# Optimization experiments

Measured on AMD Instinct MI355X. Metric: run time of the kernel, lower is better.

Reference implementation:

```python
import jax, jax.numpy as jnp
import numpy as np

TEMPERATURE = 0.07
BASE_TEMPERATURE = 0.07


def _supcon_one(feat, labels):
    # feat: [B, V, D], labels: [B]  (contrast_mode='all')
    B, V, D = feat.shape
    N = V * B
    # torch.cat(torch.unbind(feat, dim=1), dim=0): view-major ordering
    contrast = jnp.swapaxes(feat, 0, 1).reshape(N, D)  # [N, D]
    logits = jnp.einsum('nd,md->nm', contrast, contrast) / TEMPERATURE  # [N, N]
    # subtract detached row max for numerical stability
    logits = logits - jax.lax.stop_gradient(jnp.max(logits, axis=1, keepdims=True))
    pos = (labels[:, None] == labels[None, :]).astype(feat.dtype)  # [B, B]
    mask = jnp.tile(pos, (V, V))                                   # [N, N]
    logits_mask = 1.0 - jnp.eye(N, dtype=feat.dtype)               # zero out self-contrast
    mask = mask * logits_mask
    exp_logits = jnp.exp(logits) * logits_mask
    log_prob = logits - jnp.log(exp_logits.sum(axis=1, keepdims=True))
    mean_log_prob_pos = (mask * log_prob).sum(axis=1) / mask.sum(axis=1)
    return -(TEMPERATURE / BASE_TEMPERATURE) * mean_log_prob_pos.mean()


def setup_inputs() -> dict:
    key = jax.random.key(0)
    k1, k2 = jax.random.split(key)
    feat = jax.random.normal(k1, (16, 1024, 2, 128), dtype=jnp.float32)
    feat = feat / jnp.linalg.norm(feat, axis=-1, keepdims=True)  # unit-norm embeddings
    labels = jax.random.randint(k2, (16, 1024), 0, 64)
    return {"features": feat, "labels": labels}


def reference(features, labels):
    # vmap over the outer batch dim (replaces the Python loop), then mean
    losses = jax.vmap(_supcon_one)(features, labels)
    return losses.mean()
```

## Files before the change

kernel.cpp:

```cpp
#include <hip/hip_runtime.h>
#include <hip/hip_bf16.h>

#define TEMP_INV 14.285714285714286f
#define KL2E     20.60992947626f
#define NC2      (-20.60992947626f)
#define NBATCH 16
#define NROWS 2048
#define DDIM 128

typedef __attribute__((ext_vector_type(8))) short bf16x8;
typedef __attribute__((ext_vector_type(4))) float f32x4;

#define GLOAD16(g, l) \
  __builtin_amdgcn_global_load_lds((const __attribute__((address_space(1))) void*)(g), \
                                   (__attribute__((address_space(3))) void*)(l), 16, 0, 0)

__global__ __launch_bounds__(256) void cast_reorder_kernel(
    const float* __restrict__ feat, __hip_bfloat16* __restrict__ out)
{
    int t = blockIdx.x * blockDim.x + threadIdx.x;
    int e = t << 2;
    int d = e & 127;
    int v = (e >> 7) & 1;
    int i = (e >> 8) & 1023;
    int b = e >> 18;
    const float4 f = *reinterpret_cast<const float4*>(feat + e);
    union { __hip_bfloat16 h[4]; uint2 u; } o;
    o.h[0] = __float2bfloat16(f.x);
    o.h[1] = __float2bfloat16(f.y);
    o.h[2] = __float2bfloat16(f.z);
    o.h[3] = __float2bfloat16(f.w);
    size_t oe = (size_t)(((b << 11) + (v << 10) + i)) * DDIM + d;
    *reinterpret_cast<uint2*>(out + oe) = o.u;
}

__global__ __launch_bounds__(256) void supcon_main_kernel(
    const __hip_bfloat16* __restrict__ contrast,
    const int* __restrict__ labels,
    float* __restrict__ rsum_ws, float* __restrict__ ps_ws, float* __restrict__ sd_ws)
{
    __shared__ __hip_bfloat16 Bt[2][128 * DDIM];
    __shared__ int slab[1024];
    __shared__ float red_se[2][64], red_ps[2][64], red_sd[2][64];

    const int tid  = threadIdx.x;
    const int lane = tid & 63;
    const int w    = tid >> 6;
    const int wrow = w >> 1, wcol = w & 1;

    const int bid = blockIdx.x;
    const int xcd = bid & 7, idx = bid >> 3;
    const int b   = xcd * 2 + (idx >> 5);
    const int rb  = idx & 31;
    const int n0  = rb * 64;

    const __hip_bfloat16* cb = contrast + (size_t)b * NROWS * DDIM;
    const int* lb = labels + b * 1024;

    #pragma unroll
    for (int it = 0; it < 4; ++it) slab[it * 256 + tid] = lb[it * 256 + tid];

    #pragma unroll
    for (int c = 0; c < 4; ++c) {
        const int r = (c * 4 + w) * 4 + (lane >> 4);
        const int p = lane & 15;
        GLOAD16(cb + (size_t)(n0 + r) * DDIM + ((p ^ (r & 7)) << 3),
                (char*)(&Bt[1][0]) + (c * 4 + w) * 1024);
    }
    #pragma unroll
    for (int c = 0; c < 8; ++c) {
        const int r = (c * 4 + w) * 4 + (lane >> 4);
        const int p = lane & 15;
        GLOAD16(cb + (size_t)r * DDIM + ((p ^ (r & 7)) << 3),
                (char*)(&Bt[0][0]) + (c * 4 + w) * 1024);
    }
    __syncthreads();

    bf16x8 afrag[2][4];
    #pragma unroll
    for (int fr = 0; fr < 2; ++fr) {
        const int arow = wrow * 32 + fr * 16 + (lane & 15);
        #pragma unroll
        for (int ks = 0; ks < 4; ++ks) {
            const int q = ks * 4 + (lane >> 4);
            afrag[fr][ks] = *reinterpret_cast<const bf16x8*>(
                (const char*)(&Bt[1][0]) + arow * 256 + ((q ^ (arow & 7)) << 4));
        }
    }
    int rown[2][4], rowlab[2][4];
    #pragma unroll
    for (int fr = 0; fr < 2; ++fr)
        #pragma unroll
        for (int j = 0; j < 4; ++j) {
            const int n = n0 + wrow * 32 + fr * 16 + ((lane >> 4) << 2) + j;
            rown[fr][j] = n;
            rowlab[fr][j] = slab[n & 1023];
        }
    __syncthreads();

    const __hip_bfloat16* gsrc[8];
    #pragma unroll
    for (int c = 0; c < 8; ++c) {
        const int r = (c * 4 + w) * 4 + (lane >> 4);
        const int p = lane & 15;
        gsrc[c] = cb + (size_t)(128 + r) * DDIM + ((p ^ (r & 7)) << 3);
    }
    int boff[4][4];
    #pragma unroll
    for (int fc = 0; fc < 4; ++fc) {
        const int brow = wcol * 64 + fc * 16 + (lane & 15);
        #pragma unroll
        for (int ks = 0; ks < 4; ++ks) {
            const int q = ks * 4 + (lane >> 4);
            boff[fc][ks] = brow * 256 + ((q ^ (brow & 7)) << 4);
        }
    }

    float se[2][4] = {{0,0,0,0},{0,0,0,0}};
    float ps[2][4] = {{0,0,0,0},{0,0,0,0}};
    float sd[2][4] = {{0,0,0,0},{0,0,0,0}};
    const int tdiag = rb >> 1;

    for (int t = 0; t < 16; ++t) {
        const int cur = t & 1;
        if (t < 15) {
            #pragma unroll
            for (int c = 0; c < 8; ++c) {
                GLOAD16(gsrc[c], (char*)(&Bt[cur ^ 1][0]) + (c * 4 + w) * 1024);
                gsrc[c] += 128 * DDIM;
            }
        }
        const char* base = (const char*)(&Bt[cur][0]);

        f32x4 acc[2][4];
        #pragma unroll
        for (int fr = 0; fr < 2; ++fr)
            #pragma unroll
            for (int fc = 0; fc < 4; ++fc)
                acc[fr][fc] = (f32x4){0.f, 0.f, 0.f, 0.f};

        #pragma unroll
        for (int ks = 0; ks < 4; ++ks) {
            bf16x8 bfrag[4];
            #pragma unroll
            for (int fc = 0; fc < 4; ++fc)
                bfrag[fc] = *reinterpret_cast<const bf16x8*>(base + boff[fc][ks]);
            #pragma unroll
            for (int fr = 0; fr < 2; ++fr)
                #pragma unroll
                for (int fc = 0; fc < 4; ++fc)
                    acc[fr][fc] = __builtin_amdgcn_mfma_f32_16x16x32_bf16(
                        afrag[fr][ks], bfrag[fc], acc[fr][fc], 0, 0, 0);
        }

        const int m0 = t * 128;
        #pragma unroll
        for (int fc = 0; fc < 4; ++fc) {
            const int m = m0 + wcol * 64 + fc * 16 + (lane & 15);
            const int lm = slab[m & 1023];
            #pragma unroll
            for (int fr = 0; fr < 2; ++fr)
                #pragma unroll
                for (int j = 0; j < 4; ++j) {
                    const float val = acc[fr][fc][j];
                    se[fr][j] += exp2f(fmaf(val, KL2E, NC2));
                    ps[fr][j] += (lm == rowlab[fr][j]) ? val : 0.f;
                }
        }
        if (t == tdiag) {
            #pragma unroll
            for (int fc = 0; fc < 4; ++fc) {
                const int m = m0 + wcol * 64 + fc * 16 + (lane & 15);
                #pragma unroll
                for (int fr = 0; fr < 2; ++fr)
                    #pragma unroll
                    for (int j = 0; j < 4; ++j)
                        if (m == rown[fr][j]) sd[fr][j] = acc[fr][fc][j];
            }
        }
        __syncthreads();
    }

    #pragma unroll
    for (int fr = 0; fr < 2; ++fr)
        #pragma unroll
        for (int j = 0; j < 4; ++j) {
            float s = se[fr][j], P = ps[fr][j], D = sd[fr][j];
            #pragma unroll
            for (int o = 1; o < 16; o <<= 1) {
                s += __shfl_xor(s, o);
                P += __shfl_xor(P, o);
                D += __shfl_xor(D, o);
            }
            if ((lane & 15) == 0) {
                const int r = wrow * 32 + fr * 16 + ((lane >> 4) << 2) + j;
                red_se[wcol][r] = s; red_ps[wcol][r] = P; red_sd[wcol][r] = D;
            }
        }
    __syncthreads();
    if (tid < 64) {
        const int gn = b * NROWS + n0 + tid;
        rsum_ws[gn] = red_se[0][tid] + red_se[1][tid];
        ps_ws[gn]   = red_ps[0][tid] + red_ps[1][tid];
        sd_ws[gn]   = red_sd[0][tid] + red_sd[1][tid];
    }
}

__global__ __launch_bounds__(256) void finalize_kernel(
    const int* __restrict__ labels,
    const float* __restrict__ rsum_ws, const float* __restrict__ ps_ws,
    const float* __restrict__ sd_ws, float* __restrict__ out)
{
    __shared__ int cnt_s[64];
    __shared__ float wred[4];
    const int tid = threadIdx.x, lane = tid & 63, wv = tid >> 6;
    const int gid = blockIdx.x * 256 + tid;
    const int b = gid >> 11, n = gid & 2047;
    const int* lb = labels + b * 1024;

    if (tid < 64) cnt_s[tid] = 0;
    __syncthreads();
    #pragma unroll
    for (int k = 0; k < 4; ++k) atomicAdd(&cnt_s[lb[tid * 4 + k]], 1);
    __syncthreads();

    const int l = lb[n & 1023];
    const float poscnt = (float)(2 * cnt_s[l] - 1);
    const float D  = sd_ws[gid];
    const float P  = ps_ws[gid] - D;
    const float rs = rsum_ws[gid] - exp2f(fmaf(D, KL2E, NC2));
    float mlpp = P * TEMP_INV / poscnt - TEMP_INV - __logf(rs);

    #pragma unroll
    for (int o = 1; o < 64; o <<= 1) mlpp += __shfl_xor(mlpp, o);
    if (lane == 0) wred[wv] = mlpp;
    __syncthreads();
    if (tid == 0)
        atomicAdd(out, -(wred[0] + wred[1] + wred[2] + wred[3]) * (1.0f / 32768.0f));
}

extern "C" void kernel_launch(void* const* d_in, const int* in_sizes, int n_in,
                              void* d_out, int out_size, void* d_ws, size_t ws_size,
                              hipStream_t stream) {
    const float* feat = (const float*)d_in[0];
    const int* labels = (const int*)d_in[1];
    float* out = (float*)d_out;

    char* ws = (char*)d_ws;
    __hip_bfloat16* contrast = (__hip_bfloat16*)ws;
    float* rsum_ws = (float*)(ws + 8388608);
    float* ps_ws   = (float*)(ws + 8519680);
    float* sd_ws   = (float*)(ws + 8650752);

    hipMemsetAsync(d_out, 0, sizeof(float), stream);
    cast_reorder_kernel<<<4096, 256, 0, stream>>>(feat, contrast);
    supcon_main_kernel<<<512, 256, 0, stream>>>(contrast, labels, rsum_ws, ps_ws, sd_ws);
    finalize_kernel<<<128, 256, 0, stream>>>(labels, rsum_ws, ps_ws, sd_ws, out);
}
```

Measured before the change: 112.1 us.

## Split column range across blocks with per-wave private LDS streaming and atomic reduction

The main kernel is reorganized so each wave owns 16 rows and streams 16-column B tiles through its own private double-buffered LDS region. This removes block-wide __syncthreads from the inner loop. The column range is split into two halves across blocks, doubling the grid to 1024 blocks, and launch bounds now request higher occupancy. Partial row sums are combined with global atomics into a workspace that is zeroed by an extra memset. The cost is lower MFMA reuse per B fragment (one row tile per wave instead of 2x4), plus more global loads and atomics.

```diff
diff --git a/kernel.cpp b/kernel.cpp
--- a/kernel.cpp
+++ b/kernel.cpp
@@ -4,7 +4,6 @@
 #define TEMP_INV 14.285714285714286f
 #define KL2E     20.60992947626f
 #define NC2      (-20.60992947626f)
-#define NBATCH 16
 #define NROWS 2048
 #define DDIM 128
 
@@ -34,175 +33,130 @@
     *reinterpret_cast<uint2*>(out + oe) = o.u;
 }
 
-__global__ __launch_bounds__(256) void supcon_main_kernel(
+__global__ __launch_bounds__(256, 4) void supcon_main_kernel(
     const __hip_bfloat16* __restrict__ contrast,
     const int* __restrict__ labels,
     float* __restrict__ rsum_ws, float* __restrict__ ps_ws, float* __restrict__ sd_ws)
 {
-    __shared__ __hip_bfloat16 Bt[2][128 * DDIM];
+    __shared__ __align__(16) char wbuf[4][2][4096];
     __shared__ int slab[1024];
-    __shared__ float red_se[2][64], red_ps[2][64], red_sd[2][64];
 
     const int tid  = threadIdx.x;
     const int lane = tid & 63;
     const int w    = tid >> 6;
-    const int wrow = w >> 1, wcol = w & 1;
+    const int hi   = lane >> 4;
+    const int lo   = lane & 15;
 
     const int bid = blockIdx.x;
     const int xcd = bid & 7, idx = bid >> 3;
-    const int b   = xcd * 2 + (idx >> 5);
-    const int rb  = idx & 31;
+    const int b   = xcd * 2 + (idx >> 6);
+    const int rem = idx & 63;
+    const int rb  = rem >> 1, ch = rem & 1;
     const int n0  = rb * 64;
-
-    const __hip_bfloat16* cb = contrast + (size_t)b * NROWS * DDIM;
+    const int wr0 = n0 + w * 16;
+    const int cb0 = ch * 1024;
+
+    const __hip_bfloat16* cbase = contrast + (size_t)b * NROWS * DDIM;
     const int* lb = labels + b * 1024;
 
     #pragma unroll
     for (int it = 0; it < 4; ++it) slab[it * 256 + tid] = lb[it * 256 + tid];
 
-    #pragma unroll
-    for (int c = 0; c < 4; ++c) {
-        const int r = (c * 4 + w) * 4 + (lane >> 4);
-        const int p = lane & 15;
-        GLOAD16(cb + (size_t)(n0 + r) * DDIM + ((p ^ (r & 7)) << 3),
-                (char*)(&Bt[1][0]) + (c * 4 + w) * 1024);
-    }
-    #pragma unroll
-    for (int c = 0; c < 8; ++c) {
-        const int r = (c * 4 + w) * 4 + (lane >> 4);
-        const int p = lane & 15;
-        GLOAD16(cb + (size_t)r * DDIM + ((p ^ (r & 7)) << 3),
-                (char*)(&Bt[0][0]) + (c * 4 + w) * 1024);
-    }
-    __syncthreads();
-
-    bf16x8 afrag[2][4];
-    #pragma unroll
-    for (int fr = 0; fr < 2; ++fr) {
-        const int arow = wrow * 32 + fr * 16 + (lane & 15);
-        #pragma unroll
-        for (int ks = 0; ks < 4; ++ks) {
-            const int q = ks * 4 + (lane >> 4);
-            afrag[fr][ks] = *reinterpret_cast<const bf16x8*>(
-                (const char*)(&Bt[1][0]) + arow * 256 + ((q ^ (arow & 7)) << 4));
-        }
-    }
-    int rown[2][4], rowlab[2][4];
-    #pragma unroll
-    for (int fr = 0; fr < 2; ++fr)
+    char* buf0 = &wbuf[w][0][0];
+
+    #pragma unroll
+    for (int i = 0; i < 4; ++i) {
+        const int r = 4 * i + hi;
+        GLOAD16(cbase + (size_t)(wr0 + r) * DDIM + ((lo ^ (r & 7)) << 3),
+                buf0 + i * 1024);
+    }
+    asm volatile("s_waitcnt vmcnt(0)" ::: "memory");
+    __builtin_amdgcn_sched_barrier(0);
+
+    bf16x8 afrag[4];
+    int boff[4];
+    #pragma unroll
+    for (int ks = 0; ks < 4; ++ks) {
+        boff[ks] = lo * 256 + (((hi + 4 * ks) ^ (lo & 7)) << 4);
+        afrag[ks] = *reinterpret_cast<const bf16x8*>(buf0 + boff[ks]);
+    }
+    __syncthreads();
+
+    int nrow[4], rlab[4];
+    #pragma unroll
+    for (int j = 0; j < 4; ++j) {
+        nrow[j] = wr0 + hi * 4 + j;
+        rlab[j] = slab[nrow[j] & 1023];
+    }
+
+    const __hip_bfloat16* gsrc[4];
+    #pragma unroll
+    for (int i = 0; i < 4; ++i) {
+        const int r = 4 * i + hi;
+        gsrc[i] = cbase + (size_t)(cb0 + r) * DDIM + ((lo ^ (r & 7)) << 3);
+    }
+    #pragma unroll
+    for (int i = 0; i < 4; ++i) GLOAD16(gsrc[i], buf0 + i * 1024);
+    #pragma unroll
+    for (int i = 0; i < 4; ++i) GLOAD16(gsrc[i] + 16 * DDIM, buf0 + 4096 + i * 1024);
+    #pragma unroll
+    for (int i = 0; i < 4; ++i) gsrc[i] += 32 * DDIM;
+
+    float se[4] = {0, 0, 0, 0}, ps[4] = {0, 0, 0, 0}, sdg[4] = {0, 0, 0, 0};
+    const int sd_step = (wr0 - cb0) >> 4;
+
+    for (int s = 0; s < 64; ++s) {
+        char* cur = buf0 + ((s & 1) << 12);
+        asm volatile("s_waitcnt vmcnt(4)" ::: "memory");
+        __builtin_amdgcn_sched_barrier(0);
+
+        bf16x8 bf[4];
+        #pragma unroll
+        for (int ks = 0; ks < 4; ++ks)
+            bf[ks] = *reinterpret_cast<const bf16x8*>(cur + boff[ks]);
+
+        f32x4 acc = {0.f, 0.f, 0.f, 0.f};
+        #pragma unroll
+        for (int ks = 0; ks < 4; ++ks)
+            acc = __builtin_amdgcn_mfma_f32_16x16x32_bf16(afrag[ks], bf[ks], acc, 0, 0, 0);
+
+        #pragma unroll
+        for (int i = 0; i < 4; ++i) { GLOAD16(gsrc[i], cur + i * 1024); gsrc[i] += 16 * DDIM; }
+        if (s == 61) {
+            #pragma unroll
+            for (int i = 0; i < 4; ++i) gsrc[i] -= 64 * 16 * DDIM;
+        }
+
+        const int lm = slab[s * 16 + lo];
         #pragma unroll
         for (int j = 0; j < 4; ++j) {
-            const int n = n0 + wrow * 32 + fr * 16 + ((lane >> 4) << 2) + j;
-            rown[fr][j] = n;
-            rowlab[fr][j] = slab[n & 1023];
-        }
-    __syncthreads();
-
-    const __hip_bfloat16* gsrc[8];
-    #pragma unroll
-    for (int c = 0; c < 8; ++c) {
-        const int r = (c * 4 + w) * 4 + (lane >> 4);
-        const int p = lane & 15;
-        gsrc[c] = cb + (size_t)(128 + r) * DDIM + ((p ^ (r & 7)) << 3);
-    }
-    int boff[4][4];
-    #pragma unroll
-    for (int fc = 0; fc < 4; ++fc) {
-        const int brow = wcol * 64 + fc * 16 + (lane & 15);
-        #pragma unroll
-        for (int ks = 0; ks < 4; ++ks) {
-            const int q = ks * 4 + (lane >> 4);
-            boff[fc][ks] = brow * 256 + ((q ^ (brow & 7)) << 4);
-        }
-    }
-
-    float se[2][4] = {{0,0,0,0},{0,0,0,0}};
-    float ps[2][4] = {{0,0,0,0},{0,0,0,0}};
-    float sd[2][4] = {{0,0,0,0},{0,0,0,0}};
-    const int tdiag = rb >> 1;
-
-    for (int t = 0; t < 16; ++t) {
-        const int cur = t & 1;
-        if (t < 15) {
+            const float v = acc[j];
+            se[j] += exp2f(fmaf(v, KL2E, NC2));
+            ps[j] += (lm == rlab[j]) ? v : 0.f;
+        }
+        if (s == sd_step) {
+            const int m = cb0 + s * 16 + lo;
             #pragma unroll
-            for (int c = 0; c < 8; ++c) {
-                GLOAD16(gsrc[c], (char*)(&Bt[cur ^ 1][0]) + (c * 4 + w) * 1024);
-                gsrc[c] += 128 * DDIM;
-            }
-        }
-        const char* base = (const char*)(&Bt[cur][0]);
-
-        f32x4 acc[2][4];
-        #pragma unroll
-        for (int fr = 0; fr < 2; ++fr)
-            #pragma unroll
-            for (int fc = 0; fc < 4; ++fc)
-                acc[fr][fc] = (f32x4){0.f, 0.f, 0.f, 0.f};
-
-        #pragma unroll
-        for (int ks = 0; ks < 4; ++ks) {
-            bf16x8 bfrag[4];
-            #pragma unroll
-            for (int fc = 0; fc < 4; ++fc)
-                bfrag[fc] = *reinterpret_cast<const bf16x8*>(base + boff[fc][ks]);
-            #pragma unroll
-            for (int fr = 0; fr < 2; ++fr)
-                #pragma unroll
-                for (int fc = 0; fc < 4; ++fc)
-                    acc[fr][fc] = __builtin_amdgcn_mfma_f32_16x16x32_bf16(
-                        afrag[fr][ks], bfrag[fc], acc[fr][fc], 0, 0, 0);
-        }
-
-        const int m0 = t * 128;
-        #pragma unroll
-        for (int fc = 0; fc < 4; ++fc) {
-            const int m = m0 + wcol * 64 + fc * 16 + (lane & 15);
-            const int lm = slab[m & 1023];
-            #pragma unroll
-            for (int fr = 0; fr < 2; ++fr)
-                #pragma unroll
-                for (int j = 0; j < 4; ++j) {
-                    const float val = acc[fr][fc][j];
-                    se[fr][j] += exp2f(fmaf(val, KL2E, NC2));
-                    ps[fr][j] += (lm == rowlab[fr][j]) ? val : 0.f;
-                }
-        }
-        if (t == tdiag) {
-            #pragma unroll
-            for (int fc = 0; fc < 4; ++fc) {
-                const int m = m0 + wcol * 64 + fc * 16 + (lane & 15);
-                #pragma unroll
-                for (int fr = 0; fr < 2; ++fr)
-                    #pragma unroll
-                    for (int j = 0; j < 4; ++j)
-                        if (m == rown[fr][j]) sd[fr][j] = acc[fr][fc][j];
-            }
-        }
-        __syncthreads();
-    }
-
-    #pragma unroll
-    for (int fr = 0; fr < 2; ++fr)
-        #pragma unroll
-        for (int j = 0; j < 4; ++j) {
-            float s = se[fr][j], P = ps[fr][j], D = sd[fr][j];
-            #pragma unroll
-            for (int o = 1; o < 16; o <<= 1) {
-                s += __shfl_xor(s, o);
-                P += __shfl_xor(P, o);
-                D += __shfl_xor(D, o);
-            }
-            if ((lane & 15) == 0) {
-                const int r = wrow * 32 + fr * 16 + ((lane >> 4) << 2) + j;
-                red_se[wcol][r] = s; red_ps[wcol][r] = P; red_sd[wcol][r] = D;
-            }
-        }
-    __syncthreads();
-    if (tid < 64) {
-        const int gn = b * NROWS + n0 + tid;
-        rsum_ws[gn] = red_se[0][tid] + red_se[1][tid];
-        ps_ws[gn]   = red_ps[0][tid] + red_ps[1][tid];
-        sd_ws[gn]   = red_sd[0][tid] + red_sd[1][tid];
+            for (int j = 0; j < 4; ++j)
+                if (m == nrow[j]) sdg[j] = acc[j];
+        }
+    }
+
+    #pragma unroll
+    for (int j = 0; j < 4; ++j) {
+        float s = se[j], P = ps[j], D = sdg[j];
+        #pragma unroll
+        for (int o = 1; o < 16; o <<= 1) {
+            s += __shfl_xor(s, o);
+            P += __shfl_xor(P, o);
+            D += __shfl_xor(D, o);
+        }
+        if (lo == 0) {
+            const int gn = b * NROWS + nrow[j];
+            atomicAdd(&rsum_ws[gn], s);
+            atomicAdd(&ps_ws[gn], P);
+            atomicAdd(&sd_ws[gn], D);
+        }
     }
 }
 
@@ -253,7 +207,8 @@
     float* sd_ws   = (float*)(ws + 8650752);
 
     hipMemsetAsync(d_out, 0, sizeof(float), stream);
+    hipMemsetAsync(ws + 8388608, 0, 3 * 131072, stream);
     cast_reorder_kernel<<<4096, 256, 0, stream>>>(feat, contrast);
-    supcon_main_kernel<<<512, 256, 0, stream>>>(contrast, labels, rsum_ws, ps_ws, sd_ws);
+    supcon_main_kernel<<<1024, 256, 0, stream>>>(contrast, labels, rsum_ws, ps_ws, sd_ws);
     finalize_kernel<<<128, 256, 0, stream>>>(labels, rsum_ws, ps_ws, sd_ws, out);
 }
```

Result: slower. 119.5 us (+6.6%).
